# Kernel tuning notes

Hardware: AMD Instinct MI355X
Metric: run time of the kernel (lower is better)

Reference implementation:

```python
import jax, jax.numpy as jnp
import numpy as np

B, S, T, D, H = 2, 2048, 2048, 512, 8
HD = D // H
CLAMP = 1e9


def _padding_cross_mask(key):
    # emulate cross_mask(): valid prefixes for src and tgt sequences
    k1, k2 = jax.random.split(key)
    src_len = jax.random.randint(k1, (B,), S // 2, S + 1)  # [B]
    tgt_len = jax.random.randint(k2, (B,), T // 2, T + 1)  # [B]
    src_valid = jnp.arange(S)[None, :] < src_len[:, None]  # [B,S]
    tgt_valid = jnp.arange(T)[None, :] < tgt_len[:, None]  # [B,T]
    m = tgt_valid[:, :, None] & src_valid[:, None, :]      # [B,T,S]
    return m[:, None, :, :]                                 # [B,1,T,S]


def setup_inputs() -> dict:
    key = jax.random.key(0)
    ks = jax.random.split(key, 10)
    sc = 0.02
    return {
        "x": jax.random.normal(ks[0], (B, S, D), jnp.float32),
        "y": jax.random.normal(ks[1], (B, T, D), jnp.float32),
        "mask": _padding_cross_mask(ks[2]),
        "kv_w": jax.random.normal(ks[3], (D, 2 * D), jnp.float32) * sc,
        "kv_b": jax.random.normal(ks[4], (2 * D,), jnp.float32) * sc,
        "q_w": jax.random.normal(ks[5], (D, D), jnp.float32) * sc,
        "q_b": jax.random.normal(ks[6], (D,), jnp.float32) * sc,
        "o_w": jax.random.normal(ks[7], (D, D), jnp.float32) * sc,
        "o_b": jax.random.normal(ks[8], (D,), jnp.float32) * sc,
    }


def reference(x, y, mask, kv_w, kv_b, q_w, q_b, o_w, o_b):
    b, t, d = y.shape
    s = x.shape[1]
    kv = x @ kv_w + kv_b                               # [B,S,2D]
    q = y @ q_w + q_b                                  # [B,T,D]
    kv = kv.reshape(b, s, H, 2 * HD).transpose(0, 2, 1, 3)  # [B,H,S,2hd]
    q = q.reshape(b, t, H, HD).transpose(0, 2, 1, 3)        # [B,H,T,hd]
    k, v = kv[..., :HD], kv[..., HD:]
    scores = jnp.einsum("bhtd,bhsd->bhts", q, k) / jnp.sqrt(jnp.float32(HD))
    scores = jnp.where(mask, scores, -jnp.inf)
    scores = jnp.clip(scores, -CLAMP, CLAMP)
    attn = jax.nn.softmax(scores, axis=-1)             # [B,H,T,S]
    vals = jnp.einsum("bhts,bhsd->bhtd", attn, v)
    vals = vals.transpose(0, 2, 1, 3).reshape(b, t, d)
    return vals @ o_w + o_b
```

## Files before the change

kernel.cpp:

```cpp
#include <hip/hip_runtime.h>
#include <hip/hip_bf16.h>
#include <stdint.h>

#define BN 2
#define SL 2048
#define TL 2048
#define DD 512
#define HN 8
#define HDIM 64
#define NSPLIT 2
#define QSCALE 0.1803368801111f
#define MFIX 12.0f

typedef __attribute__((ext_vector_type(8))) short bf16x8;
typedef __attribute__((ext_vector_type(4))) float f32x4;

static __device__ __forceinline__ unsigned short f2bf(float f) {
    union { float f; unsigned int u; } c; c.f = f;
    unsigned int u = c.u;
    unsigned int r = (u + 0x7fffu + ((u >> 16) & 1u)) >> 16;
    return (unsigned short)r;
}

static __device__ __forceinline__ void gload_lds16(const void* g, void* l) {
    __builtin_amdgcn_global_load_lds(
        (const __attribute__((address_space(1))) unsigned int*)g,
        (__attribute__((address_space(3))) unsigned int*)l, 16, 0, 0);
}

__global__ __launch_bounds__(256) void prep_kernel(
    const float* __restrict__ x, const float* __restrict__ y,
    const float* __restrict__ kv_w, const float* __restrict__ q_w,
    const float* __restrict__ o_w, const void* __restrict__ mask,
    unsigned short* __restrict__ xb, unsigned short* __restrict__ yb,
    unsigned short* __restrict__ kvwT, unsigned short* __restrict__ qwT,
    unsigned short* __restrict__ owT, int* __restrict__ lens,
    float* __restrict__ vmean)
{
    __shared__ unsigned short lds[64][80];
    __shared__ int kind_sh;
    __shared__ int lpart[4];
    int bx = blockIdx.x;
    int tid = threadIdx.x;
    if (bx < 2048) {
        const float* src = (bx < 1024) ? x : y;
        unsigned short* dst = (bx < 1024) ? xb : yb;
        long long i = ((long long)(bx & 1023) * 256 + tid) * 8;
        float4 v0 = *(const float4*)&src[i];
        float4 v1 = *(const float4*)&src[i + 4];
        unsigned long long p0 =
            (unsigned long long)f2bf(v0.x) | ((unsigned long long)f2bf(v0.y) << 16) |
            ((unsigned long long)f2bf(v0.z) << 32) | ((unsigned long long)f2bf(v0.w) << 48);
        unsigned long long p1 =
            (unsigned long long)f2bf(v1.x) | ((unsigned long long)f2bf(v1.y) << 16) |
            ((unsigned long long)f2bf(v1.z) << 32) | ((unsigned long long)f2bf(v1.w) << 48);
        *(unsigned long long*)&dst[i] = p0;
        *(unsigned long long*)&dst[i + 4] = p1;
        return;
    }
    if (bx >= 2308) {
        float4 z = {0.f, 0.f, 0.f, 0.f};
        ((float4*)vmean)[tid] = z;
        return;
    }
    if (bx >= 2304) {
        int blk = bx - 2304;
        int b = blk >> 1, is_tgt = blk & 1;
        if (tid == 0) {
            unsigned int v = *(const unsigned int*)mask;
            int kind = 0;
            if (v == 0x01010101u) kind = 1;
            else if (v == 0x3f800000u) kind = 2;
            else if (v == 0x3f803f80u) kind = 3;
            kind_sh = kind;
        }
        __syncthreads();
        int kind = kind_sh;
        int lane = tid & 63, wid = tid >> 6;
        int cnt = 0;
        for (int i = tid; i < (is_tgt ? TL : SL); i += 256) {
            long long idx = is_tgt ? ((long long)(b * TL + i)) * SL
                                   : ((long long)(b * TL + 0)) * SL + i;
            bool bit;
            if (kind == 0)      bit = ((const int*)mask)[idx] != 0;
            else if (kind == 1) bit = ((const unsigned char*)mask)[idx] != 0;
            else if (kind == 2) bit = ((const float*)mask)[idx] != 0.0f;
            else                bit = ((const unsigned short*)mask)[idx] != 0;
            cnt += bit ? 1 : 0;
        }
        #pragma unroll
        for (int off = 32; off >= 1; off >>= 1) cnt += __shfl_xor(cnt, off, 64);
        if (lane == 0) lpart[wid] = cnt;
        __syncthreads();
        if (tid == 0)
            lens[is_tgt * 2 + b] = lpart[0] + lpart[1] + lpart[2] + lpart[3];
        return;
    }
    const float* W; unsigned short* Wt; int N, tb;
    if (bx < 2176)      { W = kv_w; Wt = kvwT; N = 1024; tb = bx - 2048; }
    else if (bx < 2240) { W = q_w;  Wt = qwT;  N = 512;  tb = bx - 2176; }
    else                { W = o_w;  Wt = owT;  N = 512;  tb = bx - 2240; }
    int nblk = N / 64;
    int n0 = (tb % nblk) * 64, k0 = (tb / nblk) * 64;
    #pragma unroll
    for (int i = 0; i < 4; ++i) {
        int fi = tid + i * 256;
        int kl = fi >> 4;
        int nl = (fi & 15) * 4;
        float4 v = *(const float4*)&W[(long long)(k0 + kl) * N + n0 + nl];
        lds[nl + 0][kl] = f2bf(v.x);
        lds[nl + 1][kl] = f2bf(v.y);
        lds[nl + 2][kl] = f2bf(v.z);
        lds[nl + 3][kl] = f2bf(v.w);
    }
    __syncthreads();
    #pragma unroll
    for (int i = 0; i < 2; ++i) {
        int fi = tid + i * 256;
        int nl = fi >> 3;
        int kl = (fi & 7) * 8;
        *(bf16x8*)&Wt[(long long)(n0 + nl) * 512 + k0 + kl] = *(const bf16x8*)&lds[nl][kl];
    }
}

static __device__ __forceinline__ void mainloop_64x128(
    const unsigned short* __restrict__ Ab, const unsigned short* __restrict__ Bt,
    int m0, int n0, int tid,
    unsigned short* Alds,
    unsigned short* Blds,
    f32x4 (&acc)[2][4])
{
    int lane = tid & 63, wid = tid >> 6;
    int wr = wid >> 1, wc = wid & 1;
    int lr = lane & 15, lg = lane >> 4;
    int rl = lane >> 2;
    int sc = (lane & 3) ^ ((rl >> 1) & 3);

    auto stage = [&](int buf, int kt) {
        #pragma unroll
        for (int j = 0; j < 3; ++j) {
            int seg = wid * 3 + j;
            if (seg < 4) {
                int row = seg * 16 + rl;
                gload_lds16(&Ab[((long long)(m0 + row)) * 512 + kt * 32 + sc * 8],
                            (char*)(Alds + buf * 2048) + seg * 1024);
            } else {
                int s2 = seg - 4;
                int row = s2 * 16 + rl;
                gload_lds16(&Bt[((long long)(n0 + row)) * 512 + kt * 32 + sc * 8],
                            (char*)(Blds + buf * 4096) + s2 * 1024);
            }
        }
    };
    auto frag = [&](const unsigned short* base, int row) -> bf16x8 {
        int slot = lg ^ ((row >> 1) & 3);
        return *(const bf16x8*)((const char*)base + row * 64 + slot * 16);
    };

    stage(0, 0);
    stage(1, 1);
    for (int kt = 0; kt < 16; ++kt) {
        int buf = kt & 3;
        if (kt < 15) asm volatile("s_waitcnt vmcnt(3)" ::: "memory");
        else         asm volatile("s_waitcnt vmcnt(0)" ::: "memory");
        __builtin_amdgcn_s_barrier();
        __builtin_amdgcn_sched_barrier(0);
        if (kt + 2 < 16) stage((kt + 2) & 3, kt + 2);
        bf16x8 bfr[4];
        #pragma unroll
        for (int ni = 0; ni < 4; ++ni)
            bfr[ni] = frag(Blds + buf * 4096, wc * 64 + ni * 16 + lr);
        #pragma unroll
        for (int mi = 0; mi < 2; ++mi) {
            bf16x8 afr = frag(Alds + buf * 2048, wr * 32 + mi * 16 + lr);
            #pragma unroll
            for (int ni = 0; ni < 4; ++ni)
                acc[mi][ni] = __builtin_amdgcn_mfma_f32_16x16x32_bf16(
                                  afr, bfr[ni], acc[mi][ni], 0, 0, 0);
        }
    }
}

__global__ __launch_bounds__(256) void gemm_kvq(
    const unsigned short* __restrict__ xb, const unsigned short* __restrict__ yb,
    const unsigned short* __restrict__ kvwT, const unsigned short* __restrict__ qwT,
    const float* __restrict__ kv_b, const float* __restrict__ q_b,
    const int* __restrict__ lens,
    unsigned short* __restrict__ Kbuf, unsigned short* __restrict__ Vtbuf,
    unsigned short* __restrict__ Qbuf, float* __restrict__ vmean)
{
    __shared__ __align__(16) unsigned short Alds[4][64 * 32];
    __shared__ __align__(16) unsigned short Blds[4][128 * 32];
    int gid = blockIdx.x;
    int swz = (gid & 7) * 96 + (gid >> 3);
    int nidx = swz % 12;
    int m0 = (swz / 12) * 64;
    bool isq = nidx >= 8;
    if (isq && (m0 & 2047) >= lens[2 + (m0 >> 11)]) return;
    const unsigned short* Ab = isq ? yb : xb;
    const unsigned short* Bt = isq ? qwT : kvwT;
    const float* bias = isq ? q_b : kv_b;
    int n0 = (isq ? (nidx - 8) : nidx) * 128;
    int tid = threadIdx.x;
    int lane = tid & 63, wid = tid >> 6;
    int wr = wid >> 1, wc = wid & 1;
    int lr = lane & 15, lg = lane >> 4;

    f32x4 acc[2][4] = {};
    mainloop_64x128(Ab, Bt, m0, n0, tid, &Alds[0][0], &Blds[0][0], acc);

    float vsum[4] = {0.f, 0.f, 0.f, 0.f};
    #pragma unroll
    for (int mi = 0; mi < 2; ++mi)
    #pragma unroll
    for (int ni = 0; ni < 4; ++ni) {
        int n = n0 + wc * 64 + ni * 16 + lr;
        int mbase = m0 + wr * 32 + mi * 16 + lg * 4;
        float bv = bias[n];
        int b = mbase >> 11;
        int s = mbase & 2047;
        if (!isq) {
            int h = n >> 7, j = n & 127;
            if (j < HDIM) {
                long long base = (((long long)(b * HN + h)) * SL + s) * HDIM + j;
                #pragma unroll
                for (int r = 0; r < 4; ++r)
                    Kbuf[base + (long long)r * HDIM] = f2bf(acc[mi][ni][r] + bv);
            } else {
                int d = j - HDIM;
                long long base = (((long long)(b * HN + h)) * HDIM + d) * SL + s;
                unsigned long long p = 0;
                #pragma unroll
                for (int r = 0; r < 4; ++r)
                    p |= (unsigned long long)f2bf(acc[mi][ni][r] + bv) << (16 * r);
                *(unsigned long long*)&Vtbuf[base] = p;
                vsum[ni] += ((acc[mi][ni][0] + bv) + (acc[mi][ni][1] + bv)) +
                            ((acc[mi][ni][2] + bv) + (acc[mi][ni][3] + bv));
            }
        } else {
            int h = n >> 6, j = n & 63;
            long long base = (((long long)(b * HN + h)) * TL + s) * HDIM + j;
            #pragma unroll
            for (int r = 0; r < 4; ++r)
                Qbuf[base + (long long)r * HDIM] = f2bf((acc[mi][ni][r] + bv) * QSCALE);
        }
    }
    if (!isq && wc == 1) {
        int bh = (m0 >> 11) * HN + (n0 >> 7);
        #pragma unroll
        for (int ni = 0; ni < 4; ++ni) {
            float v = vsum[ni];
            v += __shfl_xor(v, 16, 64);
            v += __shfl_xor(v, 32, 64);
            if (lg == 0)
                atomicAdd(&vmean[bh * HDIM + ni * 16 + lr], v * (1.0f / SL));
        }
    }
}

__global__ __launch_bounds__(256) void gemm_out(
    const unsigned short* __restrict__ Ab, const unsigned short* __restrict__ Bt,
    const float* __restrict__ bias, float* __restrict__ outF)
{
    __shared__ __align__(16) unsigned short Alds[4][64 * 32];
    __shared__ __align__(16) unsigned short Blds[4][128 * 32];
    const int N = 512;
    int n0 = blockIdx.x * 128;
    int m0 = blockIdx.y * 64;
    int tid = threadIdx.x;
    int lane = tid & 63, wid = tid >> 6;
    int wr = wid >> 1, wc = wid & 1;
    int lr = lane & 15, lg = lane >> 4;

    f32x4 acc[2][4] = {};
    mainloop_64x128(Ab, Bt, m0, n0, tid, &Alds[0][0], &Blds[0][0], acc);

    #pragma unroll
    for (int mi = 0; mi < 2; ++mi)
    #pragma unroll
    for (int ni = 0; ni < 4; ++ni) {
        int n = n0 + wc * 64 + ni * 16 + lr;
        int mbase = m0 + wr * 32 + mi * 16 + lg * 4;
        float bv = bias[n];
        #pragma unroll
        for (int r = 0; r < 4; ++r)
            outF[(long long)(mbase + r) * N + n] = acc[mi][ni][r] + bv;
    }
}

__global__ __launch_bounds__(512) void attn_kernel(
    const unsigned short* __restrict__ Q,
    const unsigned short* __restrict__ K,
    const unsigned short* __restrict__ Vt,
    const int* __restrict__ lens,
    float* __restrict__ pml,
    float* __restrict__ pacc)
{
    __shared__ unsigned short Kt[4][4096];
    __shared__ unsigned short Vl[4][4096];
    __shared__ unsigned int P32[8][16][32];
    int idx = blockIdx.x;
    int gid = (idx & 7) * 64 + (idx >> 3);
    int t0 = (gid & 15) * 128;
    int bhsp = gid >> 4;
    int bh = bhsp >> 1;
    int sp = bhsp & 1;
    int b = bh >> 3;
    int tid = threadIdx.x;
    int lane = tid & 63, wid = tid >> 6;
    int tcol = lane & 15, lg = lane >> 4;
    int t0w = t0 + wid * 16;
    int src_len = lens[b];
    int tgt_len = lens[2 + b];
    if (t0 >= tgt_len) return;

    int nsch = (src_len + 63) >> 6;
    if (nsch > SL / 64) nsch = SL / 64;
    int nch = (nsch - sp + 1) >> 1;

    const unsigned short* Qb = Q + ((long long)bh * TL) * HDIM;
    const unsigned short* Kb = K + ((long long)bh * SL) * HDIM;
    const unsigned short* Vb = Vt + ((long long)bh * HDIM) * SL;

    bf16x8 qf0 = *(const bf16x8*)&Qb[(t0w + tcol) * HDIM + lg * 8];
    bf16x8 qf1 = *(const bf16x8*)&Qb[(t0w + tcol) * HDIM + 32 + lg * 8];
    asm volatile("" : "+v"(qf0), "+v"(qf1));

    int sub = lane >> 3;
    int scol = (lane & 7) ^ sub;
    auto stage = [&](int buf, int s0) {
        int g = wid;
        int row = g * 8 + sub;
        gload_lds16(&Kb[(s0 + row) * HDIM + scol * 8],
                    (char*)&Kt[buf][0] + g * 1024);
        gload_lds16(&Vb[(long long)row * SL + s0 + scol * 8],
                    (char*)&Vl[buf][0] + g * 1024);
    };

    f32x4 accv[4] = {};
    float l_run = 0.0f;
    int pswz = (tcol & 7) << 2;

    stage(0, sp * 64);
    if (nch > 1) stage(1, (2 + sp) * 64);

    for (int c = 0; c < nch; ++c) {
        int s0 = (2 * c + sp) * 64;
        if (c + 1 < nch) asm volatile("s_waitcnt vmcnt(2)" ::: "memory");
        else             asm volatile("s_waitcnt vmcnt(0)" ::: "memory");
        __builtin_amdgcn_s_barrier();
        __builtin_amdgcn_sched_barrier(0);
        if (c + 2 < nch) stage((c + 2) & 3, (2 * (c + 2) + sp) * 64);
        const char* Kl = (const char*)&Kt[c & 3][0];
        const char* Vlb = (const char*)&Vl[c & 3][0];

        float sv[4][4];
        __builtin_amdgcn_s_setprio(1);
        #pragma unroll
        for (int st = 0; st < 4; ++st) {
            int krow = st * 16 + tcol;
            int swz = (krow & 7) << 4;
            bf16x8 kf0 = *(const bf16x8*)(Kl + krow * 128 + ((lg << 4) ^ swz));
            bf16x8 kf1 = *(const bf16x8*)(Kl + krow * 128 + (((lg + 4) << 4) ^ swz));
            f32x4 sa = {};
            sa = __builtin_amdgcn_mfma_f32_16x16x32_bf16(kf0, qf0, sa, 0, 0, 0);
            sa = __builtin_amdgcn_mfma_f32_16x16x32_bf16(kf1, qf1, sa, 0, 0, 0);
            #pragma unroll
            for (int r = 0; r < 4; ++r) sv[st][r] = sa[r];
        }
        __builtin_amdgcn_s_setprio(0);
        if (s0 + 64 > src_len) {
            #pragma unroll
            for (int st = 0; st < 4; ++st)
                #pragma unroll
                for (int r = 0; r < 4; ++r) {
                    int s = s0 + st * 16 + lg * 4 + r;
                    if (s >= src_len) sv[st][r] = -1e30f;
                }
        }
        float ps[4];
        #pragma unroll
        for (int st = 0; st < 4; ++st) {
            float p0 = __builtin_amdgcn_exp2f(sv[st][0] - MFIX);
            float p1 = __builtin_amdgcn_exp2f(sv[st][1] - MFIX);
            float p2 = __builtin_amdgcn_exp2f(sv[st][2] - MFIX);
            float p3 = __builtin_amdgcn_exp2f(sv[st][3] - MFIX);
            ps[st] = (p0 + p1) + (p2 + p3);
            unsigned int w0, w1;
            asm("v_cvt_pk_bf16_f32 %0, %1, %2" : "=v"(w0) : "v"(p0), "v"(p1));
            asm("v_cvt_pk_bf16_f32 %0, %1, %2" : "=v"(w1) : "v"(p2), "v"(p3));
            int wsw = (st * 8 + lg * 2) ^ pswz;
            *(unsigned long long*)&P32[wid][tcol][wsw] =
                (unsigned long long)w0 | ((unsigned long long)w1 << 32);
        }
        float psum = (ps[0] + ps[1]) + (ps[2] + ps[3]);
        psum += __shfl_xor(psum, 16, 64);
        psum += __shfl_xor(psum, 32, 64);
        l_run += psum;
        asm volatile("s_waitcnt lgkmcnt(0)" ::: "memory");
        __builtin_amdgcn_sched_barrier(0);
        __builtin_amdgcn_s_setprio(1);
        #pragma unroll
        for (int c2 = 0; c2 < 2; ++c2) {
            bf16x8 pf = *(const bf16x8*)&P32[wid][tcol][(c2 * 16 + lg * 4) ^ pswz];
            #pragma unroll
            for (int dc = 0; dc < 4; ++dc) {
                int vrow = dc * 16 + tcol;
                bf16x8 vf = *(const bf16x8*)(Vlb + vrow * 128 +
                                             ((((c2 * 4 + lg) << 4)) ^ ((vrow & 7) << 4)));
                accv[dc] = __builtin_amdgcn_mfma_f32_16x16x32_bf16(pf, vf, accv[dc], 0, 0, 0);
            }
        }
        __builtin_amdgcn_s_setprio(0);
    }

    #pragma unroll
    for (int dc = 0; dc < 4; ++dc)
        #pragma unroll
        for (int r = 0; r < 4; ++r) {
            long long rowidx = (long long)bh * TL + t0w + lg * 4 + r;
            pacc[(rowidx * NSPLIT + sp) * 64 + dc * 16 + tcol] = accv[dc][r];
        }
    if (lg == 0) {
        long long rowidx = (long long)bh * TL + t0w + tcol;
        pml[rowidx * NSPLIT + sp] = l_run;
    }
}

__global__ __launch_bounds__(256) void combine_kernel(
    const float* __restrict__ pml, const float* __restrict__ pacc,
    const float* __restrict__ vmean, const int* __restrict__ lens,
    unsigned short* __restrict__ valsb)
{
    int lane = threadIdx.x & 63, wid = threadIdx.x >> 6;
    const int rows_total = BN * HN * TL;
    for (int row = blockIdx.x * 4 + wid; row < rows_total; row += gridDim.x * 4) {
        int bh = row >> 11, t = row & 2047;
        int b = bh >> 3, h = bh & 7;
        float o;
        if (t >= lens[2 + b]) {
            o = vmean[bh * HDIM + lane];
        } else {
            float l = pml[row * 2 + 0] + pml[row * 2 + 1];
            float a1 = pacc[((long long)row * 2 + 0) * 64 + lane];
            float a2 = pacc[((long long)row * 2 + 1) * 64 + lane];
            o = (a1 + a2) / l;
        }
        valsb[((long long)(b * TL + t)) * DD + h * HDIM + lane] = f2bf(o);
    }
}

extern "C" void kernel_launch(void* const* d_in, const int* in_sizes, int n_in,
                              void* d_out, int out_size, void* d_ws, size_t ws_size,
                              hipStream_t stream)
{
    const float* x    = (const float*)d_in[0];
    const float* y    = (const float*)d_in[1];
    const void*  mask = d_in[2];
    const float* kv_w = (const float*)d_in[3];
    const float* kv_b = (const float*)d_in[4];
    const float* q_w  = (const float*)d_in[5];
    const float* q_b  = (const float*)d_in[6];
    const float* o_w  = (const float*)d_in[7];
    const float* o_b  = (const float*)d_in[8];
    float* out = (float*)d_out;

    char* ws = (char*)d_ws;
    int* lens = (int*)ws;
    unsigned short* Qbuf  = (unsigned short*)(ws + 256);
    unsigned short* Kbuf  = Qbuf + (size_t)2097152;
    unsigned short* Vtbuf = Kbuf + (size_t)2097152;
    float* pml  = (float*)(Vtbuf + (size_t)2097152);
    float* pacc = pml + (size_t)262144;
    unsigned short* valsb = (unsigned short*)(pacc + (size_t)4194304);
    unsigned short* kvwT = valsb + (size_t)2097152;
    unsigned short* qwT  = kvwT + (size_t)524288;
    unsigned short* owT  = qwT + (size_t)262144;
    float* vmean = (float*)(owT + (size_t)262144);
    unsigned short* xb = (unsigned short*)pacc;
    unsigned short* yb = xb + (size_t)2097152;

    prep_kernel<<<2309, 256, 0, stream>>>(x, y, kv_w, q_w, o_w, mask,
                                          xb, yb, kvwT, qwT, owT, lens, vmean);
    gemm_kvq<<<768, 256, 0, stream>>>(xb, yb, kvwT, qwT, kv_b, q_b,
                                      lens, Kbuf, Vtbuf, Qbuf, vmean);
    attn_kernel<<<512, 512, 0, stream>>>(Qbuf, Kbuf, Vtbuf, lens, pml, pacc);
    combine_kernel<<<2048, 256, 0, stream>>>(pml, pacc, vmean, lens, valsb);
    gemm_out<<<dim3(4, 64), 256, 0, stream>>>(valsb, owT, o_b, out);
}
```

Baseline: 70.24 us.

## Merge split-KV halves inside one 1024-thread block and fuse combine kernel

The two source-split halves of attention now run as two wave groups of one 1024-thread block instead of separate blocks. They reduce their partial accumulators and row sums through shared memory and write the normalized bf16 output directly, which removes the combine kernel launch and the fp32 partial-result round trip through global memory. In exchange the grid halves to 256 blocks, the K/V pipeline drops from 4-deep to double buffering with a full vmcnt(0) wait, and the shorter half must run dummy masked iterations to stay on the shared barriers. This may reduce occupancy and latency hiding.

New measurement: 65.92 us. 1.07x faster.

```diff
diff --git a/kernel.cpp b/kernel.cpp
--- a/kernel.cpp
+++ b/kernel.cpp
@@ -8,7 +8,6 @@
 #define DD 512
 #define HN 8
 #define HDIM 64
-#define NSPLIT 2
 #define QSCALE 0.1803368801111f
 #define MFIX 12.0f
 
@@ -288,35 +287,51 @@
     }
 }
 
-__global__ __launch_bounds__(512) void attn_kernel(
+__global__ __launch_bounds__(1024) void attn_kernel(
     const unsigned short* __restrict__ Q,
     const unsigned short* __restrict__ K,
     const unsigned short* __restrict__ Vt,
     const int* __restrict__ lens,
-    float* __restrict__ pml,
-    float* __restrict__ pacc)
+    const float* __restrict__ vmean,
+    unsigned short* __restrict__ valsb)
 {
-    __shared__ unsigned short Kt[4][4096];
-    __shared__ unsigned short Vl[4][4096];
-    __shared__ unsigned int P32[8][16][32];
+    __shared__ __align__(16) unsigned short KV[2][2][2][4096];
+    __shared__ unsigned int P32[16][16][32];
+    float* acc_sh = (float*)&KV[0][0][0][0];
+    float* l_sh   = (float*)&KV[1][0][0][0];
+
     int idx = blockIdx.x;
-    int gid = (idx & 7) * 64 + (idx >> 3);
+    int gid = (idx & 7) * 32 + (idx >> 3);
     int t0 = (gid & 15) * 128;
-    int bhsp = gid >> 4;
-    int bh = bhsp >> 1;
-    int sp = bhsp & 1;
-    int b = bh >> 3;
+    int bh = gid >> 4;
+    int b = bh >> 3, h = bh & 7;
     int tid = threadIdx.x;
     int lane = tid & 63, wid = tid >> 6;
+    int sp = wid >> 3, wv = wid & 7;
     int tcol = lane & 15, lg = lane >> 4;
-    int t0w = t0 + wid * 16;
+    int t0w = t0 + wv * 16;
     int src_len = lens[b];
     int tgt_len = lens[2 + b];
-    if (t0 >= tgt_len) return;
+
+    if (t0 >= tgt_len) {
+        if (sp == 0) {
+            #pragma unroll
+            for (int dc = 0; dc < 4; ++dc) {
+                unsigned short ob = f2bf(vmean[bh * HDIM + dc * 16 + tcol]);
+                #pragma unroll
+                for (int r = 0; r < 4; ++r) {
+                    int t = t0w + lg * 4 + r;
+                    valsb[((long long)(b * TL + t)) * DD + h * HDIM + dc * 16 + tcol] = ob;
+                }
+            }
+        }
+        return;
+    }
 
     int nsch = (src_len + 63) >> 6;
     if (nsch > SL / 64) nsch = SL / 64;
-    int nch = (nsch - sp + 1) >> 1;
+    int nch_own = (nsch - sp + 1) >> 1;
+    int nchmax = (nsch + 1) >> 1;
 
     const unsigned short* Qb = Q + ((long long)bh * TL) * HDIM;
     const unsigned short* Kb = K + ((long long)bh * SL) * HDIM;
@@ -329,12 +344,11 @@
     int sub = lane >> 3;
     int scol = (lane & 7) ^ sub;
     auto stage = [&](int buf, int s0) {
-        int g = wid;
-        int row = g * 8 + sub;
+        int row = wv * 8 + sub;
         gload_lds16(&Kb[(s0 + row) * HDIM + scol * 8],
-                    (char*)&Kt[buf][0] + g * 1024);
+                    (char*)&KV[sp][buf][0][0] + wv * 1024);
         gload_lds16(&Vb[(long long)row * SL + s0 + scol * 8],
-                    (char*)&Vl[buf][0] + g * 1024);
+                    (char*)&KV[sp][buf][1][0] + wv * 1024);
     };
 
     f32x4 accv[4] = {};
@@ -342,17 +356,16 @@
     int pswz = (tcol & 7) << 2;
 
     stage(0, sp * 64);
-    if (nch > 1) stage(1, (2 + sp) * 64);
-
-    for (int c = 0; c < nch; ++c) {
+
+    for (int c = 0; c < nchmax; ++c) {
         int s0 = (2 * c + sp) * 64;
-        if (c + 1 < nch) asm volatile("s_waitcnt vmcnt(2)" ::: "memory");
-        else             asm volatile("s_waitcnt vmcnt(0)" ::: "memory");
+        bool live = c < nch_own;
+        asm volatile("s_waitcnt vmcnt(0)" ::: "memory");
         __builtin_amdgcn_s_barrier();
         __builtin_amdgcn_sched_barrier(0);
-        if (c + 2 < nch) stage((c + 2) & 3, (2 * (c + 2) + sp) * 64);
-        const char* Kl = (const char*)&Kt[c & 3][0];
-        const char* Vlb = (const char*)&Vl[c & 3][0];
+        if (c + 1 < nch_own) stage((c + 1) & 1, s0 + 128);
+        const char* Kl = (const char*)&KV[sp][c & 1][0][0];
+        const char* Vlb = (const char*)&KV[sp][c & 1][1][0];
 
         float sv[4][4];
         __builtin_amdgcn_s_setprio(1);
@@ -369,7 +382,12 @@
             for (int r = 0; r < 4; ++r) sv[st][r] = sa[r];
         }
         __builtin_amdgcn_s_setprio(0);
-        if (s0 + 64 > src_len) {
+        if (!live) {
+            #pragma unroll
+            for (int st = 0; st < 4; ++st)
+                #pragma unroll
+                for (int r = 0; r < 4; ++r) sv[st][r] = -1e30f;
+        } else if (s0 + 64 > src_len) {
             #pragma unroll
             for (int st = 0; st < 4; ++st)
                 #pragma unroll
@@ -414,39 +432,34 @@
         __builtin_amdgcn_s_setprio(0);
     }
 
-    #pragma unroll
-    for (int dc = 0; dc < 4; ++dc)
-        #pragma unroll
-        for (int r = 0; r < 4; ++r) {
-            long long rowidx = (long long)bh * TL + t0w + lg * 4 + r;
-            pacc[(rowidx * NSPLIT + sp) * 64 + dc * 16 + tcol] = accv[dc][r];
-        }
-    if (lg == 0) {
-        long long rowidx = (long long)bh * TL + t0w + tcol;
-        pml[rowidx * NSPLIT + sp] = l_run;
-    }
-}
-
-__global__ __launch_bounds__(256) void combine_kernel(
-    const float* __restrict__ pml, const float* __restrict__ pacc,
-    const float* __restrict__ vmean, const int* __restrict__ lens,
-    unsigned short* __restrict__ valsb)
-{
-    int lane = threadIdx.x & 63, wid = threadIdx.x >> 6;
-    const int rows_total = BN * HN * TL;
-    for (int row = blockIdx.x * 4 + wid; row < rows_total; row += gridDim.x * 4) {
-        int bh = row >> 11, t = row & 2047;
-        int b = bh >> 3, h = bh & 7;
-        float o;
-        if (t >= lens[2 + b]) {
-            o = vmean[bh * HDIM + lane];
-        } else {
-            float l = pml[row * 2 + 0] + pml[row * 2 + 1];
-            float a1 = pacc[((long long)row * 2 + 0) * 64 + lane];
-            float a2 = pacc[((long long)row * 2 + 1) * 64 + lane];
-            o = (a1 + a2) / l;
-        }
-        valsb[((long long)(b * TL + t)) * DD + h * HDIM + lane] = f2bf(o);
+    __builtin_amdgcn_s_barrier();
+    if (sp == 1) {
+        #pragma unroll
+        for (int dc = 0; dc < 4; ++dc)
+            *(f32x4*)&acc_sh[((wv * 64 + lane) * 16) + dc * 4] = accv[dc];
+        if (lg == 0) l_sh[wv * 16 + tcol] = l_run;
+    }
+    __builtin_amdgcn_s_barrier();
+    if (sp == 0) {
+        float lo[4];
+        #pragma unroll
+        for (int r = 0; r < 4; ++r)
+            lo[r] = __shfl(l_run, lg * 4 + r, 64) + l_sh[wv * 16 + lg * 4 + r];
+        float vm[4][4];
+        #pragma unroll
+        for (int dc = 0; dc < 4; ++dc)
+            vm[dc][0] = vmean[bh * HDIM + dc * 16 + tcol];
+        #pragma unroll
+        for (int dc = 0; dc < 4; ++dc) {
+            f32x4 oth = *(const f32x4*)&acc_sh[((wv * 64 + lane) * 16) + dc * 4];
+            #pragma unroll
+            for (int r = 0; r < 4; ++r) {
+                int t = t0w + lg * 4 + r;
+                float o = (t >= tgt_len) ? vm[dc][0]
+                          : (accv[dc][r] + oth[r]) * __builtin_amdgcn_rcpf(lo[r]);
+                valsb[((long long)(b * TL + t)) * DD + h * HDIM + dc * 16 + tcol] = f2bf(o);
+            }
+        }
     }
 }
 
@@ -470,21 +483,18 @@
     unsigned short* Qbuf  = (unsigned short*)(ws + 256);
     unsigned short* Kbuf  = Qbuf + (size_t)2097152;
     unsigned short* Vtbuf = Kbuf + (size_t)2097152;
-    float* pml  = (float*)(Vtbuf + (size_t)2097152);
-    float* pacc = pml + (size_t)262144;
-    unsigned short* valsb = (unsigned short*)(pacc + (size_t)4194304);
+    unsigned short* xb = Vtbuf + (size_t)2097152;
+    unsigned short* yb = xb + (size_t)2097152;
+    unsigned short* valsb = yb + (size_t)2097152;
     unsigned short* kvwT = valsb + (size_t)2097152;
     unsigned short* qwT  = kvwT + (size_t)524288;
     unsigned short* owT  = qwT + (size_t)262144;
     float* vmean = (float*)(owT + (size_t)262144);
-    unsigned short* xb = (unsigned short*)pacc;
-    unsigned short* yb = xb + (size_t)2097152;
 
     prep_kernel<<<2309, 256, 0, stream>>>(x, y, kv_w, q_w, o_w, mask,
                                           xb, yb, kvwT, qwT, owT, lens, vmean);
     gemm_kvq<<<768, 256, 0, stream>>>(xb, yb, kvwT, qwT, kv_b, q_b,
                                       lens, Kbuf, Vtbuf, Qbuf, vmean);
-    attn_kernel<<<512, 512, 0, stream>>>(Qbuf, Kbuf, Vtbuf, lens, pml, pacc);
-    combine_kernel<<<2048, 256, 0, stream>>>(pml, pacc, vmean, lens, valsb);
+    attn_kernel<<<256, 1024, 0, stream>>>(Qbuf, Kbuf, Vtbuf, lens, vmean, valsb);
     gemm_out<<<dim3(4, 64), 256, 0, stream>>>(valsb, owT, o_b, out);
 }
```
